# Kernel tuning notes

Hardware: AMD Instinct MI355X
Metric: run time of the kernel (lower is better)

## Reference

```python
import jax, jax.numpy as jnp
import numpy as np

N_BASES = 4  # a,c,g,u
L = 4096


def setup_inputs() -> dict:
    key = jax.random.key(0)
    seq_ids = jax.random.randint(key, (L,), 0, N_BASES, dtype=jnp.int64)
    # BASE_DICT: each base -> one-hot vector of length N_BASES (identity table)
    base_table = jnp.eye(N_BASES, dtype=jnp.float32)
    return {"seq_ids": seq_ids, "base_table": base_table}


def reference(seq_ids, base_table):
    # one_hot[i] = BASE_DICT[sequence[i]]  -> (L, N_BASES)
    one_hot = base_table[seq_ids]
    n = one_hot.shape[0]
    # ret[:, i, j] = cat(one_hot[i], one_hot[j])
    row = jnp.broadcast_to(one_hot[:, None, :], (n, n, N_BASES))  # first half, varies with i
    col = jnp.broadcast_to(one_hot[None, :, :], (n, n, N_BASES))  # second half, varies with j
    ret = jnp.concatenate([row, col], axis=-1)        # (L, L, 2*N_BASES)
    ret = jnp.transpose(ret, (2, 0, 1))               # (2*N_BASES, L, L)
    return ret[None]                                  # (1, 2*N_BASES, L, L)
```

## Files before the change

kernel.cpp:

```cpp
#include <hip/hip_runtime.h>


#define L 4096
#define ROWS 4
#define ROW_F4 (L / 4)
#define PLANE_F4 (L * (L / 4))

typedef float v4f __attribute__((ext_vector_type(4)));
typedef int   v4i __attribute__((ext_vector_type(4)));

__global__ __launch_bounds__(256) void SequenceEmbedding_30923764532139_kernel(
        const int* __restrict__ seq,
        const float* __restrict__ table,
        v4f* __restrict__ out) {
    const unsigned bid   = blockIdx.x;
    const unsigned plane = bid >> 10;
    const unsigned i0    = (bid & 1023u) * ROWS;
    const unsigned t     = threadIdx.x;

    v4f* base = out + (size_t)plane * PLANE_F4 + (size_t)i0 * ROW_F4;

    if (plane < 4u) {
        const unsigned c = plane;
        float x[ROWS];
#pragma unroll
        for (int r = 0; r < ROWS; ++r)
            x[r] = table[(unsigned)seq[i0 + r] * 4u + c];

#pragma unroll
        for (int r = 0; r < ROWS; ++r) {
            const v4f val = (v4f){x[r], x[r], x[r], x[r]};
            v4f* rowp = base + (size_t)r * ROW_F4;
#pragma unroll
            for (int k = 0; k < 4; ++k)
                rowp[(unsigned)k * 256u + t] = val;
        }
    } else {
        const unsigned cc = plane - 4u;
        v4f vals[4];
#pragma unroll
        for (int k = 0; k < 4; ++k) {
            const unsigned j = (unsigned)k * 1024u + t * 4u;
            const v4i s = *(const v4i*)(seq + j);
            vals[k].x = table[(unsigned)s.x * 4u + cc];
            vals[k].y = table[(unsigned)s.y * 4u + cc];
            vals[k].z = table[(unsigned)s.z * 4u + cc];
            vals[k].w = table[(unsigned)s.w * 4u + cc];
        }

#pragma unroll
        for (int r = 0; r < ROWS; ++r) {
            v4f* rowp = base + (size_t)r * ROW_F4;
#pragma unroll
            for (int k = 0; k < 4; ++k)
                rowp[(unsigned)k * 256u + t] = vals[k];
        }
    }
}

extern "C" void kernel_launch(void* const* d_in, const int* in_sizes, int n_in,
                              void* d_out, int out_size, void* d_ws, size_t ws_size,
                              hipStream_t stream) {
    const int*   seq   = (const int*)d_in[0];
    const float* table = (const float*)d_in[1];
    v4f*         out   = (v4f*)d_out;

    dim3 block(256);
    dim3 grid(8u * (L / ROWS));
    SequenceEmbedding_30923764532139_kernel<<<grid, block, 0, stream>>>(seq, table, out);
}
```

Baseline: 525.1 us.

## Use fewer blocks that loop over strided rows per plane

Reduces the grid to 128 blocks per output plane, with each block writing 32 rows strided by 128 instead of 4 contiguous rows. This amortizes block launch and per-block setup, such as the column-value gather, over more stores. The trade-off is fewer resident waves to keep store traffic in flight, plus a loop with partial unrolling.

```diff
diff --git a/kernel.cpp b/kernel.cpp
--- a/kernel.cpp
+++ b/kernel.cpp
@@ -2,7 +2,8 @@
 
 
 #define L 4096
-#define ROWS 4
+#define BPP 128u
+#define ROWS_PER_BLOCK (L / BPP)
 #define ROW_F4 (L / 4)
 #define PLANE_F4 (L * (L / 4))
 
@@ -14,26 +15,22 @@
         const float* __restrict__ table,
         v4f* __restrict__ out) {
     const unsigned bid   = blockIdx.x;
-    const unsigned plane = bid >> 10;
-    const unsigned i0    = (bid & 1023u) * ROWS;
+    const unsigned plane = bid >> 7;
+    const unsigned slot  = bid & (BPP - 1u);
     const unsigned t     = threadIdx.x;
 
-    v4f* base = out + (size_t)plane * PLANE_F4 + (size_t)i0 * ROW_F4;
+    v4f* pbase = out + (size_t)plane * PLANE_F4;
 
     if (plane < 4u) {
-        const unsigned c = plane;
-        float x[ROWS];
-#pragma unroll
-        for (int r = 0; r < ROWS; ++r)
-            x[r] = table[(unsigned)seq[i0 + r] * 4u + c];
-
-#pragma unroll
-        for (int r = 0; r < ROWS; ++r) {
-            const v4f val = (v4f){x[r], x[r], x[r], x[r]};
-            v4f* rowp = base + (size_t)r * ROW_F4;
+#pragma unroll 4
+        for (unsigned r = 0; r < ROWS_PER_BLOCK; ++r) {
+            const unsigned row = slot + r * BPP;
+            const float x = table[(unsigned)seq[row] * 4u + plane];
+            const v4f val = (v4f){x, x, x, x};
+            v4f* rowp = pbase + (size_t)row * ROW_F4 + t;
 #pragma unroll
             for (int k = 0; k < 4; ++k)
-                rowp[(unsigned)k * 256u + t] = val;
+                rowp[(unsigned)k * 256u] = val;
         }
     } else {
         const unsigned cc = plane - 4u;
@@ -48,12 +45,13 @@
             vals[k].w = table[(unsigned)s.w * 4u + cc];
         }
 
-#pragma unroll
-        for (int r = 0; r < ROWS; ++r) {
-            v4f* rowp = base + (size_t)r * ROW_F4;
+#pragma unroll 4
+        for (unsigned r = 0; r < ROWS_PER_BLOCK; ++r) {
+            const unsigned row = slot + r * BPP;
+            v4f* rowp = pbase + (size_t)row * ROW_F4 + t;
 #pragma unroll
             for (int k = 0; k < 4; ++k)
-                rowp[(unsigned)k * 256u + t] = vals[k];
+                rowp[(unsigned)k * 256u] = vals[k];
         }
     }
 }
@@ -66,6 +64,6 @@
     v4f*         out   = (v4f*)d_out;
 
     dim3 block(256);
-    dim3 grid(8u * (L / ROWS));
+    dim3 grid(8u * BPP);
     SequenceEmbedding_30923764532139_kernel<<<grid, block, 0, stream>>>(seq, table, out);
 }
```

After: 528.0 us. Within noise of the previous version (+0.6%).
